# Performance work log

Hardware: AMD Instinct MI355X
Metric: run time of the kernel (lower is better)

The kernel has to match this reference:

```python
import jax, jax.numpy as jnp
import numpy as np

B, S, C, H = 1024, 254, 2, 1024
TIME_DIM = 64
HALF = TIME_DIM // 2
N_STEPS = 50


def time_embed(t):
    # t: [B] -> [B, 64] sinusoidal embedding, matching SinusoidalEmbedding(64)
    freqs = jnp.exp(jnp.arange(HALF, dtype=jnp.float32) * (-np.log(10000.0) / (HALF - 1)))
    ang = t[:, None] * freqs[None, :]  # [B, 32]
    return jnp.concatenate([jnp.sin(ang), jnp.cos(ang)], axis=-1)  # [B, 64]


def setup_inputs() -> dict:
    key = jax.random.key(0)
    ks = jax.random.split(key, 12)
    inp = {}
    inp["state"] = jax.random.normal(ks[0], (B, S), jnp.float32)
    inp["x0"] = jax.random.normal(ks[1], (B, C), jnp.float32)  # initial noise of sample()
    dims = [S + C + TIME_DIM, H, H, H, H, C]  # 320 -> 1024 x4 -> 2
    for i in range(5):
        kw, kb = jax.random.split(ks[2 + i])
        inp[f"W{i}"] = jax.random.normal(kw, (dims[i], dims[i + 1]), jnp.float32) * (1.0 / np.sqrt(dims[i]))
        inp[f"b{i}"] = jax.random.normal(kb, (dims[i + 1],), jnp.float32) * 0.01
    return inp


def reference(state, x0, W0, b0, W1, b1, W2, b2, W3, b3, W4, b4):
    dt = 1.0 / N_STEPS

    def velocity(x, t):
        temb = time_embed(t)
        h = jnp.concatenate([state, x, temb], axis=-1)  # [B, 320]
        h = jax.nn.silu(h @ W0 + b0)
        h = jax.nn.silu(h @ W1 + b1)
        h = jax.nn.silu(h @ W2 + b2)
        h = jax.nn.silu(h @ W3 + b3)
        return h @ W4 + b4  # [B, C]

    def step(x, i):
        t = jnp.full((state.shape[0],), i * dt, dtype=jnp.float32)
        return x + dt * velocity(x, t), None

    x, _ = jax.lax.scan(step, x0, jnp.arange(N_STEPS, dtype=jnp.float32))
    return x
```

## Files before the change

### kernel.cpp

```cpp
#include <hip/hip_runtime.h>


typedef __bf16 bf16x8 __attribute__((ext_vector_type(8)));
typedef float  f32x4  __attribute__((ext_vector_type(4)));
typedef unsigned short u16;
typedef u16 u16x8 __attribute__((ext_vector_type(8)));
typedef u16 u16x4 __attribute__((ext_vector_type(4)));

#define H 1024
#define BATCH 1024
#define SDIM 254
#define NSTEP 50
#define DT 0.02f

__device__ __forceinline__ u16 f2bf(float f) {
  unsigned int u = __float_as_uint(f);
  return (u16)((u + 0x7FFFu + ((u >> 16) & 1u)) >> 16);
}

__device__ __forceinline__ float silu(float v) {
  return v / (1.0f + __expf(-v));
}

__global__ void transpose_w(const float* __restrict__ A, const float* __restrict__ B,
                            const float* __restrict__ C, u16* __restrict__ TA,
                            u16* __restrict__ TB, u16* __restrict__ TC) {
  const float* W = (blockIdx.z == 0) ? A : (blockIdx.z == 1) ? B : C;
  u16* T = (blockIdx.z == 0) ? TA : (blockIdx.z == 1) ? TB : TC;
  __shared__ float tile[32][33];
  const int n0 = blockIdx.x * 32, k0 = blockIdx.y * 32;
  const int tx = threadIdx.x & 31, ty = threadIdx.x >> 5;
#pragma unroll
  for (int i = 0; i < 4; ++i)
    tile[ty + 8 * i][tx] = W[(k0 + ty + 8 * i) * H + n0 + tx];
  __syncthreads();
#pragma unroll
  for (int i = 0; i < 4; ++i)
    T[(size_t)(n0 + ty + 8 * i) * H + k0 + tx] = f2bf(tile[tx][ty + 8 * i]);
}

__global__ void base_gemm(const float* __restrict__ state, const float* __restrict__ W0,
                          const float* __restrict__ b0, float* __restrict__ base) {
  __shared__ float srow[8][SDIM];
  const int bx = blockIdx.x, by = blockIdx.y, tid = threadIdx.x;
  for (int i = tid; i < 8 * SDIM; i += 128)
    srow[i / SDIM][i % SDIM] = state[(size_t)(by * 8 + i / SDIM) * SDIM + i % SDIM];
  __syncthreads();
  const int n = bx * 512 + tid * 4;
  float4 bv = *(const float4*)&b0[n];
  f32x4 a[8];
#pragma unroll
  for (int r = 0; r < 8; ++r) { a[r][0] = bv.x; a[r][1] = bv.y; a[r][2] = bv.z; a[r][3] = bv.w; }
  for (int k = 0; k < SDIM; ++k) {
    float4 wv = *(const float4*)&W0[(size_t)k * H + n];
#pragma unroll
    for (int r = 0; r < 8; ++r) {
      float s = srow[r][k];
      a[r][0] += s * wv.x; a[r][1] += s * wv.y; a[r][2] += s * wv.z; a[r][3] += s * wv.w;
    }
  }
#pragma unroll
  for (int r = 0; r < 8; ++r)
    *(f32x4*)&base[(size_t)(by * 8 + r) * H + n] = a[r];
}

__global__ void tvec_kernel(const float* __restrict__ W0, float* __restrict__ tvec) {
  const int s = blockIdx.x;
  const int h = blockIdx.y * 256 + threadIdx.x;
  const float t = (float)s * DT;
  float acc = 0.0f;
#pragma unroll
  for (int j = 0; j < 32; ++j) {
    float fr = __expf((float)j * (-9.210340371976184f / 31.0f));
    float ang = t * fr;
    acc += __sinf(ang) * W0[(256 + j) * H + h] + __cosf(ang) * W0[(288 + j) * H + h];
  }
  tvec[s * H + h] = acc;
}

__global__ void init_kernel(const float* __restrict__ base, const float* __restrict__ tvec,
                            const float* __restrict__ x0, const float* __restrict__ W0,
                            u16* __restrict__ h0, float* __restrict__ xout) {
  const int b = blockIdx.x, tid = threadIdx.x;
  const float xa = x0[2 * b], xb = x0[2 * b + 1];
  if (tid == 0) { xout[2 * b] = xa; xout[2 * b + 1] = xb; }
  const int n = tid * 4;
  float4 bs = *(const float4*)&base[(size_t)b * H + n];
  float4 tv = *(const float4*)&tvec[n];
  float4 wa = *(const float4*)&W0[254 * H + n];
  float4 wb = *(const float4*)&W0[255 * H + n];
  u16x4 r;
  r[0] = f2bf(silu(bs.x + tv.x + xa * wa.x + xb * wb.x));
  r[1] = f2bf(silu(bs.y + tv.y + xa * wa.y + xb * wb.y));
  r[2] = f2bf(silu(bs.z + tv.z + xa * wa.z + xb * wb.z));
  r[3] = f2bf(silu(bs.w + tv.w + xa * wa.w + xb * wb.w));
  *(u16x4*)&h0[(size_t)b * H + n] = r;
}

__global__ __launch_bounds__(256) void gemm_mfma(const u16* __restrict__ A,
                                                 const u16* __restrict__ BT,
                                                 const float* __restrict__ bias,
                                                 void* __restrict__ out, int out_bf16) {
  __shared__ float red[4][32][68];
  const int tid = threadIdx.x;
  const int w = tid >> 6, lane = tid & 63;
  const int lr = lane & 15, quad = lane >> 4;
  const int bn = blockIdx.x, bm = blockIdx.y;

  const u16* Ap = A + (size_t)(bm * 64 + lr) * H + w * 256 + quad * 8;
  const u16* Bp = BT + (size_t)(bn * 64 + lr) * H + w * 256 + quad * 8;

  f32x4 acc[4][4] = {};
  bf16x8 fa[3][4], fb[3][4];

#define LOADSET(s, koff)                                          \
  {                                                               \
    _Pragma("unroll") for (int q = 0; q < 4; ++q) {               \
      fa[s][q] = *(const bf16x8*)(Ap + q * 16 * H + (koff));      \
      fb[s][q] = *(const bf16x8*)(Bp + q * 16 * H + (koff));      \
    }                                                             \
  }

  LOADSET(0, 0)
  LOADSET(1, 32)
#pragma unroll
  for (int it = 0; it < 8; ++it) {
    const int cur = it % 3;
    if (it < 6) {
      const int nx = (it + 2) % 3;
      LOADSET(nx, (it + 2) * 32)
    }
#pragma unroll
    for (int mt = 0; mt < 4; ++mt)
#pragma unroll
      for (int nt = 0; nt < 4; ++nt)
        acc[mt][nt] = __builtin_amdgcn_mfma_f32_16x16x32_bf16(fa[cur][mt], fb[cur][nt],
                                                              acc[mt][nt], 0, 0, 0);
  }
#undef LOADSET

  const int m = tid >> 3;
  const int n0 = (tid & 7) * 8;
#pragma unroll
  for (int half = 0; half < 2; ++half) {
    if (half) __syncthreads();
#pragma unroll
    for (int mt = 0; mt < 2; ++mt)
#pragma unroll
      for (int nt = 0; nt < 4; ++nt)
#pragma unroll
        for (int r = 0; r < 4; ++r)
          red[w][mt * 16 + quad * 4 + r][nt * 16 + lr] = acc[half * 2 + mt][nt][r];
    __syncthreads();
    const int gm = bm * 64 + half * 32 + m;
#pragma unroll
    for (int j = 0; j < 2; ++j) {
      const int n = n0 + j * 4;
      f32x4 s0 = *(const f32x4*)&red[0][m][n];
      f32x4 s1 = *(const f32x4*)&red[1][m][n];
      f32x4 s2 = *(const f32x4*)&red[2][m][n];
      f32x4 s3 = *(const f32x4*)&red[3][m][n];
      f32x4 bv = *(const f32x4*)&bias[bn * 64 + n];
      if (out_bf16) {
        u16x4 o;
#pragma unroll
        for (int r = 0; r < 4; ++r)
          o[r] = f2bf(silu(s0[r] + s1[r] + s2[r] + s3[r] + bv[r]));
        *(u16x4*)&((u16*)out)[(size_t)gm * H + bn * 64 + n] = o;
      } else {
        f32x4 o;
#pragma unroll
        for (int r = 0; r < 4; ++r)
          o[r] = silu(s0[r] + s1[r] + s2[r] + s3[r] + bv[r]);
        *(f32x4*)&((float*)out)[(size_t)gm * H + bn * 64 + n] = o;
      }
    }
  }
}

__global__ void tail_kernel(const float* __restrict__ h3, const float* __restrict__ W4,
                            const float* __restrict__ b4, float* __restrict__ x,
                            const float* __restrict__ base, const float* __restrict__ tvec,
                            const float* __restrict__ W0, u16* __restrict__ h0, int s) {
  const int b = blockIdx.x, tid = threadIdx.x;
  float s0 = 0.0f, s1 = 0.0f;
  for (int h = tid; h < H; h += 256) {
    float v = h3[(size_t)b * H + h];
    s0 += v * W4[2 * h];
    s1 += v * W4[2 * h + 1];
  }
#pragma unroll
  for (int o = 32; o > 0; o >>= 1) {
    s0 += __shfl_down(s0, o);
    s1 += __shfl_down(s1, o);
  }
  __shared__ float red[8];
  __shared__ float xs[2];
  const int w = tid >> 6;
  if ((tid & 63) == 0) { red[w * 2] = s0; red[w * 2 + 1] = s1; }
  __syncthreads();
  if (tid == 0) {
    float v0 = red[0] + red[2] + red[4] + red[6] + b4[0];
    float v1 = red[1] + red[3] + red[5] + red[7] + b4[1];
    float xa = x[2 * b] + DT * v0;
    float xb = x[2 * b + 1] + DT * v1;
    x[2 * b] = xa; x[2 * b + 1] = xb;
    xs[0] = xa; xs[1] = xb;
  }
  __syncthreads();
  if (s < NSTEP - 1) {
    const float xa = xs[0], xb = xs[1];
    const int n = tid * 4;
    float4 bs = *(const float4*)&base[(size_t)b * H + n];
    float4 tv = *(const float4*)&tvec[(size_t)(s + 1) * H + n];
    float4 wa = *(const float4*)&W0[254 * H + n];
    float4 wb = *(const float4*)&W0[255 * H + n];
    u16x4 r;
    r[0] = f2bf(silu(bs.x + tv.x + xa * wa.x + xb * wb.x));
    r[1] = f2bf(silu(bs.y + tv.y + xa * wa.y + xb * wb.y));
    r[2] = f2bf(silu(bs.z + tv.z + xa * wa.z + xb * wb.z));
    r[3] = f2bf(silu(bs.w + tv.w + xa * wa.w + xb * wb.w));
    *(u16x4*)&h0[(size_t)b * H + n] = r;
  }
}

extern "C" void kernel_launch(void* const* d_in, const int* in_sizes, int n_in,
                              void* d_out, int out_size, void* d_ws, size_t ws_size,
                              hipStream_t stream) {
  const float* state = (const float*)d_in[0];
  const float* x0    = (const float*)d_in[1];
  const float* W0    = (const float*)d_in[2];
  const float* b0    = (const float*)d_in[3];
  const float* W1    = (const float*)d_in[4];
  const float* b1    = (const float*)d_in[5];
  const float* W2    = (const float*)d_in[6];
  const float* b2    = (const float*)d_in[7];
  const float* W3    = (const float*)d_in[8];
  const float* b3    = (const float*)d_in[9];
  const float* W4    = (const float*)d_in[10];
  const float* b4    = (const float*)d_in[11];
  float* xout = (float*)d_out;

  char* ws = (char*)d_ws;
  const size_t MB = 1024 * 1024;
  float* base = (float*)(ws + 0);
  float* h3f  = (float*)(ws + 4 * MB);
  float* tvec = (float*)(ws + 8 * MB);
  u16* w1t = (u16*)(ws + 8 * MB + 256 * 1024);
  u16* w2t = (u16*)(ws + 10 * MB + 256 * 1024);
  u16* w3t = (u16*)(ws + 12 * MB + 256 * 1024);
  u16* hA  = (u16*)(ws + 14 * MB + 256 * 1024);
  u16* hB  = (u16*)(ws + 16 * MB + 256 * 1024);
  u16* hC  = (u16*)(ws + 18 * MB + 256 * 1024);

  transpose_w<<<dim3(32, 32, 3), 256, 0, stream>>>(W1, W2, W3, w1t, w2t, w3t);
  base_gemm<<<dim3(2, 128), 128, 0, stream>>>(state, W0, b0, base);
  tvec_kernel<<<dim3(NSTEP, 4), 256, 0, stream>>>(W0, tvec);
  init_kernel<<<BATCH, 256, 0, stream>>>(base, tvec, x0, W0, hA, xout);

  for (int s = 0; s < NSTEP; ++s) {
    gemm_mfma<<<dim3(16, 16), 256, 0, stream>>>(hA, w1t, b1, hB, 1);
    gemm_mfma<<<dim3(16, 16), 256, 0, stream>>>(hB, w2t, b2, hC, 1);
    gemm_mfma<<<dim3(16, 16), 256, 0, stream>>>(hC, w3t, b3, h3f, 0);
    tail_kernel<<<BATCH, 256, 0, stream>>>(h3f, W4, b4, xout, base, tvec, W0, hA, s);
  }
}
```

Baseline: 2.123 ms.

## Split GEMM K across eight waves and tile the base GEMM through LDS

New measurement: 2.013 ms. -5.2%, faster.

```diff
diff --git a/kernel.cpp b/kernel.cpp
--- a/kernel.cpp
+++ b/kernel.cpp
@@ -3,9 +3,11 @@
 
 typedef __bf16 bf16x8 __attribute__((ext_vector_type(8)));
 typedef float  f32x4  __attribute__((ext_vector_type(4)));
+typedef float  f32x2  __attribute__((ext_vector_type(2)));
 typedef unsigned short u16;
 typedef u16 u16x8 __attribute__((ext_vector_type(8)));
 typedef u16 u16x4 __attribute__((ext_vector_type(4)));
+typedef u16 u16x2 __attribute__((ext_vector_type(2)));
 
 #define H 1024
 #define BATCH 1024
@@ -39,29 +41,64 @@
     T[(size_t)(n0 + ty + 8 * i) * H + k0 + tx] = f2bf(tile[tx][ty + 8 * i]);
 }
 
-__global__ void base_gemm(const float* __restrict__ state, const float* __restrict__ W0,
-                          const float* __restrict__ b0, float* __restrict__ base) {
-  __shared__ float srow[8][SDIM];
-  const int bx = blockIdx.x, by = blockIdx.y, tid = threadIdx.x;
-  for (int i = tid; i < 8 * SDIM; i += 128)
-    srow[i / SDIM][i % SDIM] = state[(size_t)(by * 8 + i / SDIM) * SDIM + i % SDIM];
-  __syncthreads();
-  const int n = bx * 512 + tid * 4;
-  float4 bv = *(const float4*)&b0[n];
-  f32x4 a[8];
-#pragma unroll
-  for (int r = 0; r < 8; ++r) { a[r][0] = bv.x; a[r][1] = bv.y; a[r][2] = bv.z; a[r][3] = bv.w; }
-  for (int k = 0; k < SDIM; ++k) {
-    float4 wv = *(const float4*)&W0[(size_t)k * H + n];
-#pragma unroll
-    for (int r = 0; r < 8; ++r) {
-      float s = srow[r][k];
-      a[r][0] += s * wv.x; a[r][1] += s * wv.y; a[r][2] += s * wv.z; a[r][3] += s * wv.w;
-    }
-  }
-#pragma unroll
-  for (int r = 0; r < 8; ++r)
-    *(f32x4*)&base[(size_t)(by * 8 + r) * H + n] = a[r];
+__global__ __launch_bounds__(256) void base_gemm(const float* __restrict__ state,
+                                                 const float* __restrict__ W0,
+                                                 const float* __restrict__ b0,
+                                                 float* __restrict__ base) {
+  __shared__ float Sst[64][68];
+  __shared__ float Wl[64][68];
+  const int bc = blockIdx.x, br = blockIdx.y, tid = threadIdx.x;
+  const int myrow = (tid >> 4) * 4;
+  const int mycol = (tid & 15) * 4;
+  const int lr = tid >> 2;
+  const int lc = (tid & 3) * 16;
+  f32x4 acc[4] = {};
+
+  for (int kc = 0; kc < 4; ++kc) {
+    const int k0 = kc * 64;
+#pragma unroll
+    for (int j = 0; j < 8; ++j) {
+      const int k = k0 + lc + 2 * j;
+      float vx = 0.f, vy = 0.f;
+      if (k + 1 < SDIM) {
+        float2 v = *(const float2*)&state[(size_t)(br * 64 + lr) * SDIM + k];
+        vx = v.x; vy = v.y;
+      } else if (k < SDIM) {
+        vx = state[(size_t)(br * 64 + lr) * SDIM + k];
+      }
+      Sst[lr][lc + 2 * j] = vx;
+      Sst[lr][lc + 2 * j + 1] = vy;
+    }
+#pragma unroll
+    for (int j = 0; j < 4; ++j) {
+      f32x4 wv = {};
+      if (k0 + lr < SDIM)
+        wv = *(const f32x4*)&W0[(size_t)(k0 + lr) * H + bc * 64 + lc + 4 * j];
+      *(f32x4*)&Wl[lr][lc + 4 * j] = wv;
+    }
+    __syncthreads();
+#pragma unroll 4
+    for (int kk = 0; kk < 64; kk += 4) {
+      f32x4 sv[4], wv[4];
+#pragma unroll
+      for (int r = 0; r < 4; ++r) sv[r] = *(const f32x4*)&Sst[myrow + r][kk];
+#pragma unroll
+      for (int j = 0; j < 4; ++j) wv[j] = *(const f32x4*)&Wl[kk + j][mycol];
+#pragma unroll
+      for (int r = 0; r < 4; ++r)
+#pragma unroll
+        for (int j = 0; j < 4; ++j)
+          acc[r] += sv[r][j] * wv[j];
+    }
+    __syncthreads();
+  }
+
+  const f32x4 bv = *(const f32x4*)&b0[bc * 64 + mycol];
+#pragma unroll
+  for (int r = 0; r < 4; ++r) {
+    f32x4 o = acc[r] + bv;
+    *(f32x4*)&base[(size_t)(br * 64 + myrow + r) * H + bc * 64 + mycol] = o;
+  }
 }
 
 __global__ void tvec_kernel(const float* __restrict__ W0, float* __restrict__ tvec) {
@@ -97,83 +134,62 @@
   *(u16x4*)&h0[(size_t)b * H + n] = r;
 }
 
-__global__ __launch_bounds__(256) void gemm_mfma(const u16* __restrict__ A,
-                                                 const u16* __restrict__ BT,
-                                                 const float* __restrict__ bias,
-                                                 void* __restrict__ out, int out_bf16) {
-  __shared__ float red[4][32][68];
+__global__ __launch_bounds__(512, 2) void gemm_mfma(const u16* __restrict__ A,
+                                                    const u16* __restrict__ BT,
+                                                    const float* __restrict__ bias,
+                                                    void* __restrict__ out, int out_bf16) {
+  __shared__ float red[8][16][68];
   const int tid = threadIdx.x;
   const int w = tid >> 6, lane = tid & 63;
   const int lr = lane & 15, quad = lane >> 4;
   const int bn = blockIdx.x, bm = blockIdx.y;
 
-  const u16* Ap = A + (size_t)(bm * 64 + lr) * H + w * 256 + quad * 8;
-  const u16* Bp = BT + (size_t)(bn * 64 + lr) * H + w * 256 + quad * 8;
+  const u16* Ap = A + (size_t)(bm * 64 + lr) * H + w * 128 + quad * 8;
+  const u16* Bp = BT + (size_t)(bn * 64 + lr) * H + w * 128 + quad * 8;
+
+  bf16x8 fa[4][4], fb[4][4];
+#pragma unroll
+  for (int it = 0; it < 4; ++it)
+#pragma unroll
+    for (int q = 0; q < 4; ++q) {
+      fa[it][q] = *(const bf16x8*)(Ap + q * 16 * H + it * 32);
+      fb[it][q] = *(const bf16x8*)(Bp + q * 16 * H + it * 32);
+    }
 
   f32x4 acc[4][4] = {};
-  bf16x8 fa[3][4], fb[3][4];
-
-#define LOADSET(s, koff)                                          \
-  {                                                               \
-    _Pragma("unroll") for (int q = 0; q < 4; ++q) {               \
-      fa[s][q] = *(const bf16x8*)(Ap + q * 16 * H + (koff));      \
-      fb[s][q] = *(const bf16x8*)(Bp + q * 16 * H + (koff));      \
-    }                                                             \
-  }
-
-  LOADSET(0, 0)
-  LOADSET(1, 32)
-#pragma unroll
-  for (int it = 0; it < 8; ++it) {
-    const int cur = it % 3;
-    if (it < 6) {
-      const int nx = (it + 2) % 3;
-      LOADSET(nx, (it + 2) * 32)
-    }
+#pragma unroll
+  for (int it = 0; it < 4; ++it)
 #pragma unroll
     for (int mt = 0; mt < 4; ++mt)
 #pragma unroll
       for (int nt = 0; nt < 4; ++nt)
-        acc[mt][nt] = __builtin_amdgcn_mfma_f32_16x16x32_bf16(fa[cur][mt], fb[cur][nt],
+        acc[mt][nt] = __builtin_amdgcn_mfma_f32_16x16x32_bf16(fa[it][mt], fb[it][nt],
                                                               acc[mt][nt], 0, 0, 0);
-  }
-#undef LOADSET
-
-  const int m = tid >> 3;
-  const int n0 = (tid & 7) * 8;
-#pragma unroll
-  for (int half = 0; half < 2; ++half) {
-    if (half) __syncthreads();
-#pragma unroll
-    for (int mt = 0; mt < 2; ++mt)
-#pragma unroll
-      for (int nt = 0; nt < 4; ++nt)
-#pragma unroll
-        for (int r = 0; r < 4; ++r)
-          red[w][mt * 16 + quad * 4 + r][nt * 16 + lr] = acc[half * 2 + mt][nt][r];
+
+  const int m = tid >> 5;
+  const int n0 = (tid & 31) * 2;
+  const f32x2 bv = *(const f32x2*)&bias[bn * 64 + n0];
+#pragma unroll
+  for (int p = 0; p < 4; ++p) {
+    if (p) __syncthreads();
+#pragma unroll
+    for (int nt = 0; nt < 4; ++nt)
+#pragma unroll
+      for (int r = 0; r < 4; ++r)
+        red[w][quad * 4 + r][nt * 16 + lr] = acc[p][nt][r];
     __syncthreads();
-    const int gm = bm * 64 + half * 32 + m;
-#pragma unroll
-    for (int j = 0; j < 2; ++j) {
-      const int n = n0 + j * 4;
-      f32x4 s0 = *(const f32x4*)&red[0][m][n];
-      f32x4 s1 = *(const f32x4*)&red[1][m][n];
-      f32x4 s2 = *(const f32x4*)&red[2][m][n];
-      f32x4 s3 = *(const f32x4*)&red[3][m][n];
-      f32x4 bv = *(const f32x4*)&bias[bn * 64 + n];
-      if (out_bf16) {
-        u16x4 o;
-#pragma unroll
-        for (int r = 0; r < 4; ++r)
-          o[r] = f2bf(silu(s0[r] + s1[r] + s2[r] + s3[r] + bv[r]));
-        *(u16x4*)&((u16*)out)[(size_t)gm * H + bn * 64 + n] = o;
-      } else {
-        f32x4 o;
-#pragma unroll
-        for (int r = 0; r < 4; ++r)
-          o[r] = silu(s0[r] + s1[r] + s2[r] + s3[r] + bv[r]);
-        *(f32x4*)&((float*)out)[(size_t)gm * H + bn * 64 + n] = o;
-      }
+    f32x2 s = {};
+#pragma unroll
+    for (int ww = 0; ww < 8; ++ww) s += *(const f32x2*)&red[ww][m][n0];
+    const int gm = bm * 64 + p * 16 + m;
+    const float v0 = silu(s[0] + bv[0]);
+    const float v1 = silu(s[1] + bv[1]);
+    if (out_bf16) {
+      u16x2 o = {f2bf(v0), f2bf(v1)};
+      *(u16x2*)&((u16*)out)[(size_t)gm * H + bn * 64 + n0] = o;
+    } else {
+      f32x2 o = {v0, v1};
+      *(f32x2*)&((float*)out)[(size_t)gm * H + bn * 64 + n0] = o;
     }
   }
 }
@@ -254,14 +270,14 @@
   u16* hC  = (u16*)(ws + 18 * MB + 256 * 1024);
 
   transpose_w<<<dim3(32, 32, 3), 256, 0, stream>>>(W1, W2, W3, w1t, w2t, w3t);
-  base_gemm<<<dim3(2, 128), 128, 0, stream>>>(state, W0, b0, base);
+  base_gemm<<<dim3(16, 16), 256, 0, stream>>>(state, W0, b0, base);
   tvec_kernel<<<dim3(NSTEP, 4), 256, 0, stream>>>(W0, tvec);
   init_kernel<<<BATCH, 256, 0, stream>>>(base, tvec, x0, W0, hA, xout);
 
   for (int s = 0; s < NSTEP; ++s) {
-    gemm_mfma<<<dim3(16, 16), 256, 0, stream>>>(hA, w1t, b1, hB, 1);
-    gemm_mfma<<<dim3(16, 16), 256, 0, stream>>>(hB, w2t, b2, hC, 1);
-    gemm_mfma<<<dim3(16, 16), 256, 0, stream>>>(hC, w3t, b3, h3f, 0);
+    gemm_mfma<<<dim3(16, 16), 512, 0, stream>>>(hA, w1t, b1, hB, 1);
+    gemm_mfma<<<dim3(16, 16), 512, 0, stream>>>(hB, w2t, b2, hC, 1);
+    gemm_mfma<<<dim3(16, 16), 512, 0, stream>>>(hC, w3t, b3, h3f, 0);
     tail_kernel<<<BATCH, 256, 0, stream>>>(h3f, W4, b4, xout, base, tvec, W0, hA, s);
   }
 }
```
